# Kernel optimization log

Measured on AMD Instinct MI355X. Metric: run time of the kernel, lower is better.

The kernel has to match this reference:

```python
import jax, jax.numpy as jnp
import numpy as np

EPS = 1e-5
NEG_SLOPE = 0.01  # torch LeakyReLU default


def setup_inputs() -> dict:
    key = jax.random.key(0)
    k1, k2 = jax.random.split(key)
    B, C, N, OUT = 4, 256, 4096, 256
    stdv = 1.0 / np.sqrt(OUT)
    x = jax.random.normal(k1, (B, C, N), dtype=jnp.float32)
    W = jax.random.uniform(k2, (C, OUT), dtype=jnp.float32, minval=-stdv, maxval=stdv)
    gamma = jnp.ones((OUT,), dtype=jnp.float32)
    beta = jnp.zeros((OUT,), dtype=jnp.float32)
    return {"x": x, "W": W, "gamma": gamma, "beta": beta}


def reference(x, W, gamma, beta):
    # x: [B, C, N] -> xt: [B, N, C]
    xt = jnp.transpose(x, (0, 2, 1))
    # adjacency: softmax over last dim of [B, N, N] self-similarity (L2=False path)
    scores = jnp.einsum('bnc,bmc->bnm', xt, xt)
    adj = jax.nn.softmax(scores, axis=-1)
    # support: [B, N, OUT]
    support = jnp.einsum('bnc,co->bno', xt, W)
    # output: [B, OUT, N]
    out = jnp.transpose(jnp.einsum('bnm,bmo->bno', adj, support), (0, 2, 1))
    y = jnp.where(out >= 0, out, NEG_SLOPE * out)  # LeakyReLU
    # BatchNorm1d (training mode): per-channel stats over batch and spatial dims
    mean = jnp.mean(y, axis=(0, 2), keepdims=True)
    var = jnp.mean(jnp.square(y - mean), axis=(0, 2), keepdims=True)
    y_hat = (y - mean) * jax.lax.rsqrt(var + EPS)
    return gamma[None, :, None] * y_hat + beta[None, :, None]
```

## Files before the change

### kernel.cpp

```cpp
#include <hip/hip_runtime.h>

typedef _Float16 f16;
typedef _Float16 f16x2 __attribute__((ext_vector_type(2)));
typedef _Float16 f16x4 __attribute__((ext_vector_type(4)));
typedef _Float16 f16x8 __attribute__((ext_vector_type(8)));
typedef float f32x4 __attribute__((ext_vector_type(4)));
typedef float f32x16 __attribute__((ext_vector_type(16)));
typedef int i32x2 __attribute__((ext_vector_type(2)));

#define B_   4
#define C_   256
#define N_   4096
#define OUT_ 256

__device__ __forceinline__ void gld_lds16(const f16* g, f16* l) {
    __builtin_amdgcn_global_load_lds(
        (const __attribute__((address_space(1))) void*)g,
        (__attribute__((address_space(3))) void*)l, 16, 0, 0);
}

__device__ __forceinline__ i32x2 perm32(float x) {
    return __builtin_amdgcn_permlane32_swap(__float_as_int(x), __float_as_int(x), false, false);
}

__global__ __launch_bounds__(256) void k_prep(const float* __restrict__ x,
                                              const float* __restrict__ W,
                                              f16* __restrict__ xt,
                                              f16* __restrict__ Wt,
                                              float* __restrict__ stats) {
    int bid = blockIdx.x;
    int t = threadIdx.x;
    if (bid < 1024) {
        int b  = bid >> 8;
        int ct = (bid >> 6) & 3;
        int nt = bid & 63;
        int c0 = ct * 64, n0 = nt * 64;
        __shared__ float tile[64][65];
        int nl = t & 63;
        int r0 = t >> 6;
        #pragma unroll
        for (int i = 0; i < 16; ++i) {
            int cl = i * 4 + r0;
            tile[cl][nl] = x[((b * C_ + c0 + cl) * N_) + n0 + nl];
        }
        __syncthreads();
        #pragma unroll
        for (int i = 0; i < 16; ++i) {
            int nl2 = i * 4 + r0;
            int cl2 = nl;
            xt[((b * N_ + n0 + nl2) * C_) + c0 + cl2] = (f16)tile[cl2][nl2];
        }
    } else {
        int wb = bid - 1024;
        #pragma unroll
        for (int i = 0; i < 4; ++i) {
            int idx = wb * 1024 + i * 256 + t;
            int c = idx >> 8, o = idx & 255;
            Wt[o * C_ + c] = (f16)W[idx];
        }
        if (wb < 2) stats[wb * 256 + t] = 0.f;
    }
}

__global__ __launch_bounds__(256) void k_support(const f16* __restrict__ xt,
                                                 const f16* __restrict__ Wt,
                                                 f16* __restrict__ supT) {
    int bid0 = blockIdx.x;
    int bid = (bid0 & 7) * 128 + (bid0 >> 3);
    int b  = bid >> 8;
    int ot = (bid >> 6) & 3;
    int mt = bid & 63;
    int o0 = ot * 64, m0 = mt * 64;
    __shared__ __align__(16) f16 Ws[64][264];
    __shared__ __align__(16) f16 Xs[64][264];
    int t = threadIdx.x;
    int wave = t >> 6, lane = t & 63, q = lane >> 4, l15 = lane & 15;
    #pragma unroll
    for (int p = 0; p < 8; ++p) {
        int idx = p * 256 + t;
        int row = idx >> 5, ch = (idx & 31) * 8;
        *(uint4*)&Ws[row][ch] = *(const uint4*)&Wt[(o0 + row) * C_ + ch];
        *(uint4*)&Xs[row][ch] = *(const uint4*)&xt[((b * N_) + m0 + row) * C_ + ch];
    }
    __syncthreads();
    f32x4 acc[4] = {};
    #pragma unroll
    for (int kk = 0; kk < 8; ++kk) {
        f16x8 a = *(f16x8*)&Ws[16 * wave + l15][kk * 32 + q * 8];
        #pragma unroll
        for (int ct = 0; ct < 4; ++ct) {
            f16x8 bb = *(f16x8*)&Xs[16 * ct + l15][kk * 32 + q * 8];
            acc[ct] = __builtin_amdgcn_mfma_f32_16x16x32_f16(a, bb, acc[ct], 0, 0, 0);
        }
    }
    #pragma unroll
    for (int ct = 0; ct < 4; ++ct)
        #pragma unroll
        for (int r = 0; r < 4; ++r) {
            int og = o0 + 16 * wave + q * 4 + r;
            int mg = m0 + 16 * ct + l15;
            supT[((b * OUT_ + og) * N_) + mg] = (f16)acc[ct][r];
        }
}

__global__ __launch_bounds__(256) __attribute__((amdgpu_waves_per_eu(2, 2)))
void k_flash(const f16* __restrict__ xt,
             const f16* __restrict__ supT,
             f16* __restrict__ Op,
             float* __restrict__ Ml) {
    int bid0 = blockIdx.x;
    int wg = (bid0 & 7) * 64 + (bid0 >> 3);
    int h  = wg >> 8;
    int b  = (wg >> 6) & 3;
    int n0 = (wg & 63) * 64;

    __shared__ __align__(16) f16 KsL[2][64 * 256];
    __shared__ __align__(16) f16 Ps[64][72];
    __shared__ float Lh[2][64];
    __shared__ float Lt[64];

    int t = threadIdx.x;
    int wave = t >> 6, lane = t & 63;
    int q = lane >> 4, l15 = lane & 15;
    int l31 = lane & 31, hi = lane >> 5;
    int nh = wave & 1, mh = wave >> 1;

    const f16* qbase = xt + ((size_t)(b * N_) + n0 + 32 * nh + l31) * C_ + 8 * hi;
    f16x8 qf[16];
    #pragma unroll
    for (int kc = 0; kc < 16; ++kc)
        qf[kc] = *(const f16x8*)&qbase[16 * kc];

    float m_fix;
    {
        float s = 0.f;
        #pragma unroll
        for (int kc = 0; kc < 16; ++kc)
            #pragma unroll
            for (int j = 0; j < 8; ++j) {
                float v = (float)qf[kc][j];
                s += v * v;
            }
        i32x2 rr = perm32(s);
        m_fix = __int_as_float(rr[0]) + __int_as_float(rr[1]);
    }

    f32x4 oacc[4][4] = {};
    float l_run = 0.f;

    const f16* kbase = xt + (size_t)b * N_ * C_;
    int c16 = (lane & 31) * 8;
    int rhalf = lane >> 5;
    int soff[8];
    #pragma unroll
    for (int j = 0; j < 8; ++j) {
        int row = wave * 16 + j * 2 + rhalf;
        soff[j] = row * 256 + (c16 ^ ((row & 7) << 3));
    }
    int swr = (l31 & 7) << 3;

    const f16* vbbase = supT + ((size_t)(b * OUT_) + 64 * wave + l15) * N_ + q * 8;

    {
        const f16* kt = kbase + (size_t)(h * 2048) * C_;
        #pragma unroll
        for (int j = 0; j < 8; ++j)
            gld_lds16(kt + soff[j], &KsL[0][wave * 4096 + j * 512]);
    }

    int cur = 0;
    for (int it = 0; it < 32; ++it) {
        int m0 = h * 2048 + it * 64;

        __syncthreads();

        f16x8 vf[2][4];
        const f16* vb = vbbase + m0;
        #pragma unroll
        for (int ks = 0; ks < 2; ++ks)
            #pragma unroll
            for (int ot = 0; ot < 4; ++ot)
                vf[ks][ot] = *(const f16x8*)&vb[(size_t)(16 * ot) * N_ + ks * 32];

        if (it < 31) {
            const f16* kt = kbase + (size_t)(m0 + 64) * C_;
            #pragma unroll
            for (int j = 0; j < 8; ++j)
                gld_lds16(kt + soff[j], &KsL[cur ^ 1][wave * 4096 + j * 512]);
        }

        f32x16 sacc = {};
        const f16* krow = &KsL[cur][(32 * mh + l31) * 256];
        __builtin_amdgcn_s_setprio(1);
        #pragma unroll
        for (int kc = 0; kc < 16; ++kc) {
            int col = (16 * kc + 8 * hi) ^ swr;
            f16x8 kf = *(const f16x8*)&krow[col];
            sacc = __builtin_amdgcn_mfma_f32_32x32x16_f16(kf, qf[kc], sacc, 0, 0, 0);
        }
        __builtin_amdgcn_s_setprio(0);

        float p[16];
        #pragma unroll
        for (int r = 0; r < 16; ++r)
            p[r] = __expf(sacc[r] - m_fix);
        float s0 = (p[0] + p[1]) + (p[2] + p[3]);
        float s1 = (p[4] + p[5]) + (p[6] + p[7]);
        float s2 = (p[8] + p[9]) + (p[10] + p[11]);
        float s3 = (p[12] + p[13]) + (p[14] + p[15]);
        l_run += (s0 + s1) + (s2 + s3);

        #pragma unroll
        for (int g = 0; g < 4; ++g) {
            f16x4 pk = { (f16)p[4 * g], (f16)p[4 * g + 1],
                         (f16)p[4 * g + 2], (f16)p[4 * g + 3] };
            *(f16x4*)&Ps[32 * nh + l31][32 * mh + 8 * g + 4 * hi] = pk;
        }

        asm volatile("s_waitcnt lgkmcnt(0)" ::: "memory");
        __builtin_amdgcn_s_barrier();
        __builtin_amdgcn_sched_barrier(0);

        __builtin_amdgcn_s_setprio(1);
        #pragma unroll
        for (int ks = 0; ks < 2; ++ks) {
            f16x8 af[4];
            #pragma unroll
            for (int nt = 0; nt < 4; ++nt)
                af[nt] = *(f16x8*)&Ps[16 * nt + l15][ks * 32 + q * 8];
            #pragma unroll
            for (int nt = 0; nt < 4; ++nt)
                #pragma unroll
                for (int ot = 0; ot < 4; ++ot)
                    oacc[nt][ot] = __builtin_amdgcn_mfma_f32_16x16x32_f16(af[nt], vf[ks][ot], oacc[nt][ot], 0, 0, 0);
        }
        __builtin_amdgcn_s_setprio(0);
        cur ^= 1;
    }

    {
        i32x2 rr = perm32(l_run);
        l_run = __int_as_float(rr[0]) + __int_as_float(rr[1]);
    }
    __syncthreads();
    if (lane < 32) Lh[mh][32 * nh + l31] = l_run;
    __syncthreads();
    if (t < 64) {
        float lt = Lh[0][t] + Lh[1][t];
        Lt[t] = 1.0f / fmaxf(lt, 1e-37f);
        Ml[(size_t)wg * 64 + t] = lt;
    }
    __syncthreads();

    float4 lv[4];
    #pragma unroll
    for (int nt = 0; nt < 4; ++nt)
        lv[nt] = *(const float4*)&Lt[16 * nt + 4 * q];

    f16* Obase = Op + (size_t)wg * (64 * 256);
    #pragma unroll
    for (int nt = 0; nt < 4; ++nt)
        #pragma unroll
        for (int ot = 0; ot < 4; ++ot)
            #pragma unroll
            for (int r = 0; r < 4; ++r) {
                int n = 16 * nt + q * 4 + r;
                int o = 64 * wave + 16 * ot + l15;
                Obase[n * 256 + o] = (f16)(oacc[nt][ot][r] * ((const float*)&lv[nt])[r]);
            }
}

__global__ __launch_bounds__(256) void k_merge(const f16* __restrict__ Op,
                                               const float* __restrict__ Ml,
                                               float* __restrict__ out,
                                               float* __restrict__ stats) {
    int bid = blockIdx.x;
    int b  = bid >> 6;
    int n0 = (bid & 63) * 64;
    int t = threadIdx.x;
    const f16* O1 = Op + (size_t)bid * (64 * 256);
    const f16* O2 = Op + (size_t)(bid + 256) * (64 * 256);
    const float* Ml1 = Ml + (size_t)bid * 64;
    const float* Ml2 = Ml + (size_t)(bid + 256) * 64;
    __shared__ float c1s[64], c2s[64];
    __shared__ float tile[256][65];
    if (t < 64) {
        float l1 = Ml1[t], l2 = Ml2[t];
        float inv = 1.0f / (l1 + l2);
        c1s[t] = l1 * inv;
        c2s[t] = l2 * inv;
    }
    __syncthreads();
    int p2 = (t & 127) * 2;
    int nh = (t >> 7) * 32;
    float s0 = 0.f, s1 = 0.f, ss0 = 0.f, ss1 = 0.f;
    #pragma unroll 8
    for (int j = 0; j < 32; ++j) {
        int n = nh + j;
        f16x2 u1 = *(const f16x2*)&O1[n * 256 + p2];
        f16x2 u2 = *(const f16x2*)&O2[n * 256 + p2];
        float c1 = c1s[n], c2 = c2s[n];
        float v0 = c1 * (float)u1[0] + c2 * (float)u2[0];
        float v1 = c1 * (float)u1[1] + c2 * (float)u2[1];
        v0 = v0 >= 0.f ? v0 : 0.01f * v0;
        v1 = v1 >= 0.f ? v1 : 0.01f * v1;
        s0 += v0; ss0 += v0 * v0;
        s1 += v1; ss1 += v1 * v1;
        tile[p2][n] = v0;
        tile[p2 + 1][n] = v1;
    }
    atomicAdd(&stats[p2], s0);
    atomicAdd(&stats[p2 + 1], s1);
    atomicAdd(&stats[256 + p2], ss0);
    atomicAdd(&stats[257 + p2], ss1);
    __syncthreads();
    int w = t >> 6, lane = t & 63;
    float* dst = out + (size_t)(b * OUT_) * N_ + n0;
    #pragma unroll
    for (int k = 0; k < 64; ++k) {
        int o = 64 * w + k;
        dst[(size_t)o * N_ + lane] = tile[o][lane];
    }
}

__global__ __launch_bounds__(256) void k_bnapply(float* __restrict__ y,
                                                 const float* __restrict__ stats,
                                                 const float* __restrict__ gamma,
                                                 const float* __restrict__ beta) {
    int idx = blockIdx.x * 256 + threadIdx.x;
    int o = (idx >> 10) & 255;
    float mean = stats[o] * (1.0f / 16384.0f);
    float var = stats[256 + o] * (1.0f / 16384.0f) - mean * mean;
    float rstd = rsqrtf(var + 1e-5f);
    float g = gamma[o] * rstd;
    float bta = beta[o] - mean * g;
    float4 v = ((const float4*)y)[idx];
    v.x = v.x * g + bta;
    v.y = v.y * g + bta;
    v.z = v.z * g + bta;
    v.w = v.w * g + bta;
    ((float4*)y)[idx] = v;
}

extern "C" void kernel_launch(void* const* d_in, const int* in_sizes, int n_in,
                              void* d_out, int out_size, void* d_ws, size_t ws_size,
                              hipStream_t stream) {
    const float* x     = (const float*)d_in[0];
    const float* W     = (const float*)d_in[1];
    const float* gamma = (const float*)d_in[2];
    const float* beta  = (const float*)d_in[3];
    float* out = (float*)d_out;

    f16* xt    = (f16*)d_ws;
    f16* supT  = xt + (size_t)B_ * N_ * C_;
    f16* Wt    = supT + (size_t)B_ * N_ * OUT_;
    f16* Op    = Wt + C_ * OUT_;
    float* Ml  = (float*)(Op + (size_t)2 * 256 * 64 * 256);
    float* stats = Ml + 512 * 128;

    k_prep<<<1088, 256, 0, stream>>>(x, W, xt, Wt, stats);
    k_support<<<1024, 256, 0, stream>>>(xt, Wt, supT);
    k_flash<<<512, 256, 0, stream>>>(xt, supT, Op, Ml);
    k_merge<<<256, 256, 0, stream>>>(Op, Ml, out, stats);
    k_bnapply<<<4096, 256, 0, stream>>>(out, stats, gamma, beta);
}
```

Before: 201.9 us.

## Single-buffer K tile in flash kernel, vectorize transpose stores, split merge grid

The flash kernel drops its double-buffered K LDS tile for a single buffer and raises the waves-per-EU hint from 2 to 3 to allow more resident waves. The next K load is now issued only after the score phase has finished reading the tile, and each iteration waits for it at the top, so that load is exposed rather than overlapped. The prep transpose writes f16x4 vectors instead of scalar halves. The merge kernel is split across four output-channel quarters (1024 blocks) with a block-level reduction before the atomics, giving more parallelism and fewer atomics per block.

```diff
diff --git a/kernel.cpp b/kernel.cpp
--- a/kernel.cpp
+++ b/kernel.cpp
@@ -45,10 +45,12 @@
         }
         __syncthreads();
         #pragma unroll
-        for (int i = 0; i < 16; ++i) {
-            int nl2 = i * 4 + r0;
-            int cl2 = nl;
-            xt[((b * N_ + n0 + nl2) * C_) + c0 + cl2] = (f16)tile[cl2][nl2];
+        for (int i = 0; i < 4; ++i) {
+            int n  = i * 16 + (t >> 4);
+            int c4 = (t & 15) * 4;
+            f16x4 o = { (f16)tile[c4][n], (f16)tile[c4 + 1][n],
+                        (f16)tile[c4 + 2][n], (f16)tile[c4 + 3][n] };
+            *(f16x4*)&xt[((b * N_ + n0 + n) * C_) + c0 + c4] = o;
         }
     } else {
         int wb = bid - 1024;
@@ -103,7 +105,7 @@
         }
 }
 
-__global__ __launch_bounds__(256) __attribute__((amdgpu_waves_per_eu(2, 2)))
+__global__ __launch_bounds__(256) __attribute__((amdgpu_waves_per_eu(3, 3)))
 void k_flash(const f16* __restrict__ xt,
              const f16* __restrict__ supT,
              f16* __restrict__ Op,
@@ -114,7 +116,7 @@
     int b  = (wg >> 6) & 3;
     int n0 = (wg & 63) * 64;
 
-    __shared__ __align__(16) f16 KsL[2][64 * 256];
+    __shared__ __align__(16) f16 KsL[64 * 256];
     __shared__ __align__(16) f16 Ps[64][72];
     __shared__ float Lh[2][64];
     __shared__ float Lt[64];
@@ -165,14 +167,15 @@
         const f16* kt = kbase + (size_t)(h * 2048) * C_;
         #pragma unroll
         for (int j = 0; j < 8; ++j)
-            gld_lds16(kt + soff[j], &KsL[0][wave * 4096 + j * 512]);
-    }
-
-    int cur = 0;
+            gld_lds16(kt + soff[j], &KsL[wave * 4096 + j * 512]);
+    }
+
     for (int it = 0; it < 32; ++it) {
         int m0 = h * 2048 + it * 64;
 
-        __syncthreads();
+        asm volatile("s_waitcnt vmcnt(0) lgkmcnt(0)" ::: "memory");
+        __builtin_amdgcn_s_barrier();
+        __builtin_amdgcn_sched_barrier(0);
 
         f16x8 vf[2][4];
         const f16* vb = vbbase + m0;
@@ -182,15 +185,8 @@
             for (int ot = 0; ot < 4; ++ot)
                 vf[ks][ot] = *(const f16x8*)&vb[(size_t)(16 * ot) * N_ + ks * 32];
 
-        if (it < 31) {
-            const f16* kt = kbase + (size_t)(m0 + 64) * C_;
-            #pragma unroll
-            for (int j = 0; j < 8; ++j)
-                gld_lds16(kt + soff[j], &KsL[cur ^ 1][wave * 4096 + j * 512]);
-        }
-
         f32x16 sacc = {};
-        const f16* krow = &KsL[cur][(32 * mh + l31) * 256];
+        const f16* krow = &KsL[(32 * mh + l31) * 256];
         __builtin_amdgcn_s_setprio(1);
         #pragma unroll
         for (int kc = 0; kc < 16; ++kc) {
@@ -221,6 +217,13 @@
         __builtin_amdgcn_s_barrier();
         __builtin_amdgcn_sched_barrier(0);
 
+        if (it < 31) {
+            const f16* kt = kbase + (size_t)(m0 + 64) * C_;
+            #pragma unroll
+            for (int j = 0; j < 8; ++j)
+                gld_lds16(kt + soff[j], &KsL[wave * 4096 + j * 512]);
+        }
+
         __builtin_amdgcn_s_setprio(1);
         #pragma unroll
         for (int ks = 0; ks < 2; ++ks) {
@@ -235,7 +238,6 @@
                     oacc[nt][ot] = __builtin_amdgcn_mfma_f32_16x16x32_f16(af[nt], vf[ks][ot], oacc[nt][ot], 0, 0, 0);
         }
         __builtin_amdgcn_s_setprio(0);
-        cur ^= 1;
     }
 
     {
@@ -274,16 +276,20 @@
                                                const float* __restrict__ Ml,
                                                float* __restrict__ out,
                                                float* __restrict__ stats) {
-    int bid = blockIdx.x;
-    int b  = bid >> 6;
-    int n0 = (bid & 63) * 64;
+    int bid0 = blockIdx.x;
+    int bid = (bid0 & 7) * 128 + (bid0 >> 3);
+    int b  = bid >> 8;
+    int nb = (bid >> 2) & 63;
+    int oq = bid & 3;
+    int n0 = nb * 64, o0 = oq * 64;
     int t = threadIdx.x;
-    const f16* O1 = Op + (size_t)bid * (64 * 256);
-    const f16* O2 = Op + (size_t)(bid + 256) * (64 * 256);
-    const float* Ml1 = Ml + (size_t)bid * 64;
-    const float* Ml2 = Ml + (size_t)(bid + 256) * 64;
+    const f16* O1 = Op + (size_t)(b * 64 + nb) * (64 * 256);
+    const f16* O2 = Op + (size_t)(b * 64 + nb + 256) * (64 * 256);
+    const float* Ml1 = Ml + (size_t)(b * 64 + nb) * 64;
+    const float* Ml2 = Ml + (size_t)(b * 64 + nb + 256) * 64;
     __shared__ float c1s[64], c2s[64];
-    __shared__ float tile[256][65];
+    __shared__ float tile[64][65];
+    __shared__ float rs[8][64], rss[8][64];
     if (t < 64) {
         float l1 = Ml1[t], l2 = Ml2[t];
         float inv = 1.0f / (l1 + l2);
@@ -291,14 +297,14 @@
         c2s[t] = l2 * inv;
     }
     __syncthreads();
-    int p2 = (t & 127) * 2;
-    int nh = (t >> 7) * 32;
+    int ow = (t & 31) * 2;
+    int ng = t >> 5;
     float s0 = 0.f, s1 = 0.f, ss0 = 0.f, ss1 = 0.f;
-    #pragma unroll 8
-    for (int j = 0; j < 32; ++j) {
-        int n = nh + j;
-        f16x2 u1 = *(const f16x2*)&O1[n * 256 + p2];
-        f16x2 u2 = *(const f16x2*)&O2[n * 256 + p2];
+    #pragma unroll
+    for (int j = 0; j < 8; ++j) {
+        int n = ng * 8 + j;
+        f16x2 u1 = *(const f16x2*)&O1[n * 256 + o0 + ow];
+        f16x2 u2 = *(const f16x2*)&O2[n * 256 + o0 + ow];
         float c1 = c1s[n], c2 = c2s[n];
         float v0 = c1 * (float)u1[0] + c2 * (float)u2[0];
         float v1 = c1 * (float)u1[1] + c2 * (float)u2[1];
@@ -306,19 +312,24 @@
         v1 = v1 >= 0.f ? v1 : 0.01f * v1;
         s0 += v0; ss0 += v0 * v0;
         s1 += v1; ss1 += v1 * v1;
-        tile[p2][n] = v0;
-        tile[p2 + 1][n] = v1;
-    }
-    atomicAdd(&stats[p2], s0);
-    atomicAdd(&stats[p2 + 1], s1);
-    atomicAdd(&stats[256 + p2], ss0);
-    atomicAdd(&stats[257 + p2], ss1);
-    __syncthreads();
+        tile[ow][n] = v0;
+        tile[ow + 1][n] = v1;
+    }
+    rs[ng][ow] = s0;  rs[ng][ow + 1] = s1;
+    rss[ng][ow] = ss0; rss[ng][ow + 1] = ss1;
+    __syncthreads();
+    if (t < 64) {
+        float S = 0.f, SS = 0.f;
+        #pragma unroll
+        for (int g = 0; g < 8; ++g) { S += rs[g][t]; SS += rss[g][t]; }
+        atomicAdd(&stats[o0 + t], S);
+        atomicAdd(&stats[256 + o0 + t], SS);
+    }
     int w = t >> 6, lane = t & 63;
-    float* dst = out + (size_t)(b * OUT_) * N_ + n0;
-    #pragma unroll
-    for (int k = 0; k < 64; ++k) {
-        int o = 64 * w + k;
+    float* dst = out + ((size_t)(b * OUT_ + o0)) * N_ + n0;
+    #pragma unroll
+    for (int k = 0; k < 16; ++k) {
+        int o = 16 * w + k;
         dst[(size_t)o * N_ + lane] = tile[o][lane];
     }
 }
@@ -361,6 +372,6 @@
     k_prep<<<1088, 256, 0, stream>>>(x, W, xt, Wt, stats);
     k_support<<<1024, 256, 0, stream>>>(xt, Wt, supT);
     k_flash<<<512, 256, 0, stream>>>(xt, supT, Op, Ml);
-    k_merge<<<256, 256, 0, stream>>>(Op, Ml, out, stats);
+    k_merge<<<1024, 256, 0, stream>>>(Op, Ml, out, stats);
     k_bnapply<<<4096, 256, 0, stream>>>(out, stats, gamma, beta);
 }
```

After: 342.5 us. 69.6% more time.
